# Optimization experiments

Measured on AMD Instinct MI355X. Metric: run time of the kernel, lower is better.

Reference implementation:

```python
import jax, jax.numpy as jnp
import numpy as np

# dims: batch, seq, d_model, d_hidden, routed experts, top-k, shared experts
B, S, D, H, E_R, K, E_S = 2, 1024, 1024, 512, 64, 6, 2
EPS = 1.1920929e-07  # torch.finfo(float32).eps, RMSNorm default when eps=None


def setup_inputs() -> dict:
    key = jax.random.key(0)
    ks = jax.random.split(key, 8)
    u = lambda k, shape, b: jax.random.uniform(k, shape, jnp.float32, -b, b)
    bd = 1.0 / np.sqrt(D)   # bound for W1 (1/sqrt(d_input)) and W2 (1/sqrt(d_output)=1/sqrt(D))
    bh = 1.0 / np.sqrt(H)
    return {
        "x": jax.random.normal(ks[0], (B, S, D), jnp.float32),
        "norm_w": jnp.ones((D,), jnp.float32),            # RMSNorm weight
        "Wr": u(ks[1], (E_R, D), bd),                      # router Linear weight (no bias)
        "sW1": u(ks[2], (E_S, D, H), bd), "sb1": jnp.zeros((E_S, 1, H), jnp.float32),
        "sW2": u(ks[3], (E_S, H, D), bd), "sb2": jnp.zeros((E_S, 1, D), jnp.float32),
        "sWg": u(ks[4], (H, H), bh),                       # shared-experts SwiGLU gate weight
        "rW1": u(ks[5], (E_R, D, H), bd), "rb1": jnp.zeros((E_R, 1, H), jnp.float32),
        "rW2": u(ks[6], (E_R, H, D), bd), "rb2": jnp.zeros((E_R, 1, D), jnp.float32),
        "rWg": u(ks[7], (H, H), bh),                       # routed-experts SwiGLU gate weight
        "bias": jnp.full((E_R,), 1.0 / E_R, jnp.float32), # routing bias buffer (expert_bias=True)
    }


def _rmsnorm(x, w):
    ms = jnp.mean(x * x, axis=-1, keepdims=True)
    return x * jax.lax.rsqrt(ms + EPS) * w


def _swiglu(h, Wg):
    # SwiGLU(d_model=H): silu(h @ Wg) * h, elementwise gate over hidden dim
    return jax.nn.silu(h @ Wg) * h


def reference(x, norm_w, Wr, sW1, sb1, sW2, sb2, sWg, rW1, rb1, rW2, rb2, rWg, bias):
    xn = _rmsnorm(x, norm_w)
    t = xn.reshape(-1, D)                                  # (T, D) tokens
    # --- shared experts, summed over expert axis ---
    hs = jnp.einsum('td,edh->teh', t, sW1) + sb1[None, :, 0, :]
    hs = _swiglu(hs, sWg)
    shared = jnp.einsum('teh,ehd->td', hs, sW2) + jnp.sum(sb2[:, 0, :], axis=0)
    # --- router ---
    raw = t @ Wr.T                                         # (T, E_R) raw affinity
    aff = jax.lax.stop_gradient(raw) + bias                # detached + bias for top-k selection
    _, idx = jax.lax.top_k(aff, K)                         # (T, K)
    # --- routed experts: dense all-expert FFN, gather top-k outputs ---
    # (mathematically identical to the source's per-token weight gather,
    #  but avoids materializing (T,K,D,H) weight tensors)
    h = jnp.einsum('td,edh->teh', t, rW1) + rb1[None, :, 0, :]   # (T, E_R, H)
    h = _swiglu(h, rWg)
    out_all = jnp.einsum('teh,ehd->ted', h, rW2) + rb2[None, :, 0, :]  # (T, E_R, D)
    out_k = jnp.take_along_axis(out_all, idx[:, :, None], axis=1)      # (T, K, D)
    aff_k = jnp.take_along_axis(raw, idx, axis=1)                      # (T, K) raw (undetached)
    w = aff_k / jnp.sum(aff_k, axis=-1, keepdims=True)                 # expert_bias=True path
    routed = jnp.einsum('tk,tkd->td', w, out_k)                        # (T, D)
    return x + (shared + routed).reshape(B, S, D)
```

## Files before the change

kernel.cpp:

```cpp
#include <hip/hip_runtime.h>
#include <cstdint>
#include <cstddef>

typedef unsigned short u16;
typedef unsigned int u32;
typedef __attribute__((ext_vector_type(8))) short bh8;
typedef __attribute__((ext_vector_type(4))) float fx4;

#define T_TOK 2048
#define D_DIM 1024
#define H_DIM 512
#define N_EXP 64
#define K_TOP 6
#define N_ASG (T_TOK * K_TOP)
#define R_TOT (N_ASG + 2 * T_TOK)
#define GRID_E (8 * 9 * 64)

__device__ __forceinline__ float bf2f(u16 v) {
    union { u32 u; float f; } c; c.u = ((u32)v) << 16; return c.f;
}
__device__ __forceinline__ u16 f2bf(float f) {
    union { u32 u; float f; } c; c.f = f;
    u32 u = c.u;
    return (u16)((u + 0x7fffu + ((u >> 16) & 1u)) >> 16);
}

__global__ __launch_bounds__(256) void rn4_k(
    const float* __restrict__ x, const float* __restrict__ nw,
    const float* __restrict__ Wr, float* __restrict__ raw, u16* __restrict__ xnb)
{
    int t0 = blockIdx.x << 2, tid = threadIdx.x;
    __shared__ float xs[4][D_DIM];
    __shared__ float ps[4][256];
    __shared__ float red4[4][4];
    int d0 = tid << 2;
    float4 wv = *(const float4*)(nw + d0);
    float4 xv[4];
    #pragma unroll
    for (int tt = 0; tt < 4; ++tt) {
        xv[tt] = *(const float4*)(x + (size_t)(t0 + tt) * D_DIM + d0);
        float ss = xv[tt].x * xv[tt].x + xv[tt].y * xv[tt].y
                 + xv[tt].z * xv[tt].z + xv[tt].w * xv[tt].w;
        #pragma unroll
        for (int o = 32; o > 0; o >>= 1) ss += __shfl_down(ss, o);
        if ((tid & 63) == 0) red4[tt][tid >> 6] = ss;
    }
    __syncthreads();
    #pragma unroll
    for (int tt = 0; tt < 4; ++tt) {
        float ms = (red4[tt][0] + red4[tt][1] + red4[tt][2] + red4[tt][3]) * (1.f / (float)D_DIM);
        float sc = rsqrtf(ms + 1.1920929e-07f);
        float4 xf;
        xf.x = xv[tt].x * sc * wv.x;
        xf.y = xv[tt].y * sc * wv.y;
        xf.z = xv[tt].z * sc * wv.z;
        xf.w = xv[tt].w * sc * wv.w;
        *(float4*)&xs[tt][d0] = xf;
        ushort4 ob;
        ob.x = f2bf(xf.x); ob.y = f2bf(xf.y); ob.z = f2bf(xf.z); ob.w = f2bf(xf.w);
        *(ushort4*)(xnb + (size_t)(t0 + tt) * D_DIM + d0) = ob;
    }
    __syncthreads();
    int e = tid & 63, part = tid >> 6;
    const float* wr = Wr + (size_t)e * D_DIM + part * 256;
    float s0 = 0.f, s1 = 0.f, s2 = 0.f, s3 = 0.f;
    const float* xp0 = &xs[0][part * 256];
    const float* xp1 = &xs[1][part * 256];
    const float* xp2 = &xs[2][part * 256];
    const float* xp3 = &xs[3][part * 256];
    #pragma unroll 4
    for (int i = 0; i < 256; i += 4) {
        float4 w4 = *(const float4*)(wr + i);
        s0 += xp0[i] * w4.x + xp0[i+1] * w4.y + xp0[i+2] * w4.z + xp0[i+3] * w4.w;
        s1 += xp1[i] * w4.x + xp1[i+1] * w4.y + xp1[i+2] * w4.z + xp1[i+3] * w4.w;
        s2 += xp2[i] * w4.x + xp2[i+1] * w4.y + xp2[i+2] * w4.z + xp2[i+3] * w4.w;
        s3 += xp3[i] * w4.x + xp3[i+1] * w4.y + xp3[i+2] * w4.z + xp3[i+3] * w4.w;
    }
    ps[0][tid] = s0; ps[1][tid] = s1; ps[2][tid] = s2; ps[3][tid] = s3;
    __syncthreads();
    if (part == 0) {
        #pragma unroll
        for (int tt = 0; tt < 4; ++tt)
            raw[(size_t)(t0 + tt) * N_EXP + e] =
                ps[tt][e] + ps[tt][64 + e] + ps[tt][128 + e] + ps[tt][192 + e];
    }
}

__global__ void topk_k(const float* __restrict__ raw, const float* __restrict__ ebias,
                       int* __restrict__ cnt, int* __restrict__ tki, float* __restrict__ tkw)
{
    int t = blockIdx.x, lane = threadIdx.x;
    float r = raw[(size_t)t * N_EXP + lane];
    float cur = r + ebias[lane];
    int selI[K_TOP]; float selR[K_TOP];
    #pragma unroll
    for (int k = 0; k < K_TOP; ++k) {
        float v = cur; int id = lane;
        #pragma unroll
        for (int o = 32; o > 0; o >>= 1) {
            float v2 = __shfl_down(v, o); int i2 = __shfl_down(id, o);
            if (v2 > v || (v2 == v && i2 < id)) { v = v2; id = i2; }
        }
        id = __shfl(id, 0);
        if (lane == id) cur = -3.4e38f;
        selI[k] = id;
        selR[k] = __shfl(r, id);
    }
    float s = 0.f;
    #pragma unroll
    for (int k = 0; k < K_TOP; ++k) s += selR[k];
    if (lane < K_TOP) {
        tki[t * K_TOP + lane] = selI[lane];
        tkw[t * K_TOP + lane] = selR[lane] / s;
        atomicAdd(&cnt[selI[lane]], 1);
    }
}

__global__ void scan_k(const int* __restrict__ cnt, int* __restrict__ offs, int* __restrict__ fill)
{
    int lane = threadIdx.x;
    int c = cnt[lane];
    int s = c;
    #pragma unroll
    for (int o = 1; o < 64; o <<= 1) {
        int v = __shfl_up(s, o);
        if (lane >= o) s += v;
    }
    int excl = s - c;
    offs[lane] = excl;
    fill[lane] = excl;
    if (lane == 63) offs[N_EXP] = s;
}

__global__ void fill_k(const int* __restrict__ tki, const float* __restrict__ tkw,
                       int* __restrict__ fill, int* __restrict__ atok, float* __restrict__ aw)
{
    int t = blockIdx.x, lane = threadIdx.x;
    if (lane < K_TOP) {
        int e = tki[t * K_TOP + lane];
        int p = atomicAdd(&fill[e], 1);
        atok[p] = t;
        aw[p] = tkw[t * K_TOP + lane];
    }
}

__global__ __launch_bounds__(256) void convAll_k(
    const float* __restrict__ rW1, const float* __restrict__ sW1,
    const float* __restrict__ rW2, const float* __restrict__ sW2,
    const float* __restrict__ rWg, const float* __restrict__ sWg,
    u16* __restrict__ W1f, u16* __restrict__ W2f, u16* __restrict__ Wgf)
{
    int id = blockIdx.x;
    const float* src; u16* dst;
    int K, N, n0, k0;
    const size_t MS = (size_t)H_DIM * D_DIM;
    if (id < 66 * 128) {
        int mat = id >> 7, tile = id & 127;
        K = D_DIM; N = H_DIM;
        src = (mat < N_EXP ? rW1 + (size_t)mat * MS : sW1 + (size_t)(mat - N_EXP) * MS);
        dst = W1f + (size_t)mat * MS;
        n0 = (tile & 7) << 6; k0 = (tile >> 3) << 6;
    } else if (id < 2 * 66 * 128) {
        id -= 66 * 128;
        int mat = id >> 7, tile = id & 127;
        K = H_DIM; N = D_DIM;
        src = (mat < N_EXP ? rW2 + (size_t)mat * MS : sW2 + (size_t)(mat - N_EXP) * MS);
        dst = W2f + (size_t)mat * MS;
        n0 = (tile & 15) << 6; k0 = (tile >> 4) << 6;
    } else {
        id -= 2 * 66 * 128;
        int mat = id >> 6, tile = id & 63;
        K = H_DIM; N = H_DIM;
        src = (mat == 0 ? rWg : sWg);
        dst = Wgf + (size_t)mat * (H_DIM * H_DIM);
        n0 = (tile & 7) << 6; k0 = (tile >> 3) << 6;
    }

    __shared__ u16 t[64][72];
    int tid = threadIdx.x;
    int kr = tid >> 4, c4 = (tid & 15) << 2;
    #pragma unroll
    for (int rr = 0; rr < 4; ++rr) {
        int k = (rr << 4) + kr;
        float4 v = *(const float4*)(src + (size_t)(k0 + k) * N + n0 + c4);
        t[c4 + 0][k] = f2bf(v.x);
        t[c4 + 1][k] = f2bf(v.y);
        t[c4 + 2][k] = f2bf(v.z);
        t[c4 + 3][k] = f2bf(v.w);
    }
    __syncthreads();
    int lane = tid & 63, g = tid >> 6;
    int nr = lane & 15, kq = lane >> 4;
    #pragma unroll
    for (int f = 0; f < 2; ++f) {
        int fragId = g + (f << 2);
        int ntile = fragId >> 1, kb = fragId & 1;
        bh8 v = *(const bh8*)&t[(ntile << 4) + nr][(kb << 5) + (kq << 3)];
        size_t fi = (((size_t)((n0 >> 4) + ntile) * (size_t)(K >> 5)
                      + (size_t)((k0 >> 5) + kb)) << 9) + (size_t)(lane << 3);
        *(bh8*)(dst + fi) = v;
    }
}

__device__ __forceinline__ bool slabDecode(
    int bx, const int* __restrict__ offs,
    int& e, int& rowBase, int& rows, int& tokBase)
{
    int xcd = bx & 7, rest = bx >> 3, grp = rest >> 6, slab = rest & 63;
    if (grp < 8) {
        e = (grp << 3) + xcd;
        int s0 = offs[e], s1 = offs[e + 1];
        rowBase = s0 + (slab << 5);
        if (rowBase >= s1) return false;
        rows = s1 - rowBase; if (rows > 32) rows = 32;
        tokBase = -1;
        return true;
    }
    int f = (slab << 3) + xcd;
    if (f >= 128) return false;
    int sh = f & 1;
    e = N_EXP + sh;
    tokBase = (f >> 1) << 5;
    rowBase = N_ASG + (sh << 11) + tokBase;
    rows = 32;
    return true;
}

__global__ __launch_bounds__(256, 4) void p1_k(
    const u16* __restrict__ xnb, const u16* __restrict__ W1f,
    const float* __restrict__ rb1, const float* __restrict__ sb1,
    const int* __restrict__ offs, const int* __restrict__ atok,
    u16* __restrict__ h)
{
    int e, rowBase, rows, tokBase;
    if (!slabDecode(blockIdx.x, offs, e, rowBase, rows, tokBase)) return;

    __shared__ int tok[32];
    int tid = threadIdx.x;
    if (tid < 32) {
        int cl = tid < rows ? tid : rows - 1;
        tok[tid] = (tokBase < 0) ? atok[rowBase + cl] : tokBase + tid;
    }
    __syncthreads();

    int w = tid >> 6, lane = tid & 63, quad = lane >> 4, l15 = lane & 15;
    int cg = blockIdx.y;
    int nt0 = (cg << 4) + (w << 2);
    const u16* bp = W1f + (size_t)e * (H_DIM * D_DIM)
                  + (((size_t)nt0 << 5) << 9) + (lane << 3);
    const u16* a0p = xnb + (size_t)tok[l15] * D_DIM + (quad << 3);
    const u16* a1p = xnb + (size_t)tok[16 + l15] * D_DIM + (quad << 3);
    const float* b1 = (tokBase < 0) ? rb1 + e * H_DIM : sb1 + (e - N_EXP) * H_DIM;

    fx4 ac0[4] = {}, ac1[4] = {};
    bh8 bA[4], bB[4], aA0, aA1, aB0, aB1;
    #pragma unroll
    for (int ct = 0; ct < 4; ++ct) bA[ct] = *(const bh8*)(bp + ((size_t)(ct << 5) << 9));
    aA0 = *(const bh8*)a0p; aA1 = *(const bh8*)a1p;
    #pragma unroll 1
    for (int kb = 0; kb < 32; kb += 2) {
        #pragma unroll
        for (int ct = 0; ct < 4; ++ct) bB[ct] = *(const bh8*)(bp + (((ct << 5) + kb + 1) << 9));
        aB0 = *(const bh8*)(a0p + ((kb + 1) << 5));
        aB1 = *(const bh8*)(a1p + ((kb + 1) << 5));
        #pragma unroll
        for (int ct = 0; ct < 4; ++ct) {
            ac0[ct] = __builtin_amdgcn_mfma_f32_16x16x32_bf16(aA0, bA[ct], ac0[ct], 0, 0, 0);
            ac1[ct] = __builtin_amdgcn_mfma_f32_16x16x32_bf16(aA1, bA[ct], ac1[ct], 0, 0, 0);
        }
        #pragma unroll
        for (int ct = 0; ct < 4; ++ct) bA[ct] = *(const bh8*)(bp + (((ct << 5) + kb + 2) << 9));
        aA0 = *(const bh8*)(a0p + ((kb + 2) << 5));
        aA1 = *(const bh8*)(a1p + ((kb + 2) << 5));
        #pragma unroll
        for (int ct = 0; ct < 4; ++ct) {
            ac0[ct] = __builtin_amdgcn_mfma_f32_16x16x32_bf16(aB0, bB[ct], ac0[ct], 0, 0, 0);
            ac1[ct] = __builtin_amdgcn_mfma_f32_16x16x32_bf16(aB1, bB[ct], ac1[ct], 0, 0, 0);
        }
    }
    #pragma unroll
    for (int ct = 0; ct < 4; ++ct) {
        int col = ((nt0 + ct) << 4) + l15;
        float bv = b1[col];
        #pragma unroll
        for (int r = 0; r < 4; ++r) {
            int r0 = (quad << 2) + r;
            if (r0 < rows) h[(size_t)(rowBase + r0) * H_DIM + col] = f2bf(ac0[ct][r] + bv);
            int r1 = 16 + r0;
            if (r1 < rows) h[(size_t)(rowBase + r1) * H_DIM + col] = f2bf(ac1[ct][r] + bv);
        }
    }
}

__global__ __launch_bounds__(256, 4) void p2_k(
    const u16* __restrict__ hbuf, const u16* __restrict__ Wgf, u16* __restrict__ hg)
{
    int rowBase = blockIdx.x << 5;
    int tid = threadIdx.x;
    int w = tid >> 6, lane = tid & 63, quad = lane >> 4, l15 = lane & 15;
    int cg = blockIdx.y;
    int nt0 = (cg << 4) + (w << 2);
    const u16* bp = Wgf + (rowBase < N_ASG ? 0 : (size_t)(H_DIM * H_DIM))
                  + (((size_t)nt0 << 4) << 9) + (lane << 3);
    const u16* a0p = hbuf + (size_t)(rowBase + l15) * H_DIM + (quad << 3);
    const u16* a1p = hbuf + (size_t)(rowBase + 16 + l15) * H_DIM + (quad << 3);

    fx4 ac0[4] = {}, ac1[4] = {};
    bh8 bA[4], bB[4], aA0, aA1, aB0, aB1;
    #pragma unroll
    for (int ct = 0; ct < 4; ++ct) bA[ct] = *(const bh8*)(bp + ((size_t)(ct << 4) << 9));
    aA0 = *(const bh8*)a0p; aA1 = *(const bh8*)a1p;
    #pragma unroll 1
    for (int kb = 0; kb < 16; kb += 2) {
        #pragma unroll
        for (int ct = 0; ct < 4; ++ct) bB[ct] = *(const bh8*)(bp + (((ct << 4) + kb + 1) << 9));
        aB0 = *(const bh8*)(a0p + ((kb + 1) << 5));
        aB1 = *(const bh8*)(a1p + ((kb + 1) << 5));
        #pragma unroll
        for (int ct = 0; ct < 4; ++ct) {
            ac0[ct] = __builtin_amdgcn_mfma_f32_16x16x32_bf16(aA0, bA[ct], ac0[ct], 0, 0, 0);
            ac1[ct] = __builtin_amdgcn_mfma_f32_16x16x32_bf16(aA1, bA[ct], ac1[ct], 0, 0, 0);
        }
        #pragma unroll
        for (int ct = 0; ct < 4; ++ct) bA[ct] = *(const bh8*)(bp + (((ct << 4) + kb + 2) << 9));
        aA0 = *(const bh8*)(a0p + ((kb + 2) << 5));
        aA1 = *(const bh8*)(a1p + ((kb + 2) << 5));
        #pragma unroll
        for (int ct = 0; ct < 4; ++ct) {
            ac0[ct] = __builtin_amdgcn_mfma_f32_16x16x32_bf16(aB0, bB[ct], ac0[ct], 0, 0, 0);
            ac1[ct] = __builtin_amdgcn_mfma_f32_16x16x32_bf16(aB1, bB[ct], ac1[ct], 0, 0, 0);
        }
    }
    #pragma unroll
    for (int ct = 0; ct < 4; ++ct) {
        int col = ((nt0 + ct) << 4) + l15;
        #pragma unroll
        for (int r = 0; r < 4; ++r) {
            int r0 = (quad << 2) + r;
            size_t i0 = (size_t)(rowBase + r0) * H_DIM + col;
            float g0 = ac0[ct][r], h0 = bf2f(hbuf[i0]);
            hg[i0] = f2bf(h0 * g0 * (1.f / (1.f + __expf(-g0))));
            int r1 = 16 + r0;
            size_t i1 = (size_t)(rowBase + r1) * H_DIM + col;
            float g1 = ac1[ct][r], h1 = bf2f(hbuf[i1]);
            hg[i1] = f2bf(h1 * g1 * (1.f / (1.f + __expf(-g1))));
        }
    }
}

__global__ __launch_bounds__(256, 4) void p3_k(
    const u16* __restrict__ hg, const u16* __restrict__ W2f,
    const float* __restrict__ rb2, const float* __restrict__ sb2,
    const int* __restrict__ offs, const int* __restrict__ atok,
    const float* __restrict__ aw, float* __restrict__ accG)
{
    int e, rowBase, rows, tokBase;
    if (!slabDecode(blockIdx.x, offs, e, rowBase, rows, tokBase)) return;

    __shared__ int tok[32];
    __shared__ float wt[32];
    int tid = threadIdx.x;
    if (tid < 32) {
        int cl = tid < rows ? tid : rows - 1;
        if (tokBase < 0) { tok[tid] = atok[rowBase + cl]; wt[tid] = aw[rowBase + cl]; }
        else             { tok[tid] = tokBase + tid;      wt[tid] = 1.0f; }
    }
    __syncthreads();

    int w = tid >> 6, lane = tid & 63, quad = lane >> 4, l15 = lane & 15;
    int cg = blockIdx.y;
    int nt0 = (cg << 4) + (w << 2);
    const u16* bp = W2f + (size_t)e * (H_DIM * D_DIM)
                  + (((size_t)nt0 << 4) << 9) + (lane << 3);
    const u16* a0p = hg + (size_t)(rowBase + l15) * H_DIM + (quad << 3);
    const u16* a1p = hg + (size_t)(rowBase + 16 + l15) * H_DIM + (quad << 3);
    const float* b2 = (tokBase < 0) ? rb2 + e * D_DIM : sb2 + (e - N_EXP) * D_DIM;

    fx4 ac0[4] = {}, ac1[4] = {};
    bh8 bA[4], bB[4], aA0, aA1, aB0, aB1;
    #pragma unroll
    for (int ct = 0; ct < 4; ++ct) bA[ct] = *(const bh8*)(bp + ((size_t)(ct << 4) << 9));
    aA0 = *(const bh8*)a0p; aA1 = *(const bh8*)a1p;
    #pragma unroll 1
    for (int kb = 0; kb < 16; kb += 2) {
        #pragma unroll
        for (int ct = 0; ct < 4; ++ct) bB[ct] = *(const bh8*)(bp + (((ct << 4) + kb + 1) << 9));
        aB0 = *(const bh8*)(a0p + ((kb + 1) << 5));
        aB1 = *(const bh8*)(a1p + ((kb + 1) << 5));
        #pragma unroll
        for (int ct = 0; ct < 4; ++ct) {
            ac0[ct] = __builtin_amdgcn_mfma_f32_16x16x32_bf16(aA0, bA[ct], ac0[ct], 0, 0, 0);
            ac1[ct] = __builtin_amdgcn_mfma_f32_16x16x32_bf16(aA1, bA[ct], ac1[ct], 0, 0, 0);
        }
        #pragma unroll
        for (int ct = 0; ct < 4; ++ct) bA[ct] = *(const bh8*)(bp + (((ct << 4) + kb + 2) << 9));
        aA0 = *(const bh8*)(a0p + ((kb + 2) << 5));
        aA1 = *(const bh8*)(a1p + ((kb + 2) << 5));
        #pragma unroll
        for (int ct = 0; ct < 4; ++ct) {
            ac0[ct] = __builtin_amdgcn_mfma_f32_16x16x32_bf16(aB0, bB[ct], ac0[ct], 0, 0, 0);
            ac1[ct] = __builtin_amdgcn_mfma_f32_16x16x32_bf16(aB1, bB[ct], ac1[ct], 0, 0, 0);
        }
    }
    #pragma unroll
    for (int ct = 0; ct < 4; ++ct) {
        int col = ((nt0 + ct) << 4) + l15;
        float bv = b2[col];
        #pragma unroll
        for (int r = 0; r < 4; ++r) {
            int r0 = (quad << 2) + r;
            if (r0 < rows)
                atomicAdd(&accG[(size_t)tok[r0] * D_DIM + col], wt[r0] * (ac0[ct][r] + bv));
            int r1 = 16 + r0;
            if (r1 < rows)
                atomicAdd(&accG[(size_t)tok[r1] * D_DIM + col], wt[r1] * (ac1[ct][r] + bv));
        }
    }
}

template<int ROUTED>
__global__ __launch_bounds__(256) void moe_ffn_k(
    const u16* __restrict__ xnb,
    const float* __restrict__ W1b, const float* __restrict__ Wg,
    const float* __restrict__ W2b,
    const float* __restrict__ b1b, const float* __restrict__ b2b,
    const int* __restrict__ offs, const int* __restrict__ atok,
    const float* __restrict__ aw, float* __restrict__ accG)
{
    int e = blockIdx.z;
    int start = ROUTED ? offs[e] : 0;
    int end   = ROUTED ? offs[e + 1] : T_TOK;
    int rowBase = start + (blockIdx.y << 5);
    if (rowBase >= end) return;
    int rows = end - rowBase; if (rows > 32) rows = 32;

    __shared__ int   tok[32];
    __shared__ float wt[32];
    __shared__ u16 hA[32 * 520];
    __shared__ u16 hG[32 * 520];
    __shared__ u16 As[32 * 32];
    __shared__ u16 Bs[64 * 36];

    int tid = threadIdx.x;
    if (tid < 32) {
        int cl = rowBase + tid; if (cl >= end) cl = end - 1;
        tok[tid] = ROUTED ? atok[cl] : cl;
        wt[tid]  = ROUTED ? aw[cl] : 1.0f;
    }
    __syncthreads();

    const float* W1 = W1b + (size_t)e * (D_DIM * H_DIM);
    const float* W2 = W2b + (size_t)e * (D_DIM * H_DIM);
    const float* b1 = b1b + e * H_DIM;
    const float* b2 = b2b + e * D_DIM;

    int w = tid >> 6, lane = tid & 63, quad = lane >> 4, l15 = lane & 15;
    int sr2 = tid >> 3, sc2 = (tid & 7) << 2;

    for (int nc = 0; nc < 8; ++nc) {
        int n0 = nc << 6;
        fx4 a0 = {}; fx4 a1 = {};
        for (int kc = 0; kc < 32; ++kc) {
            int kb = kc << 5;
            int2 av = *(const int2*)(xnb + (size_t)tok[sr2] * D_DIM + kb + sc2);
            const float* cp = W1 + n0 + lane;
            int kx = kb + (w << 3);
            u32 p[4];
            #pragma unroll
            for (int jj = 0; jj < 4; ++jj) {
                u32 lo = f2bf(cp[(size_t)(kx + 2 * jj) * H_DIM]);
                u32 hi = f2bf(cp[(size_t)(kx + 2 * jj + 1) * H_DIM]);
                p[jj] = lo | (hi << 16);
            }
            __syncthreads();
            *(int2*)&As[sr2 * 32 + sc2] = av;
            u16* bsw = &Bs[lane * 36 + (w << 3)];
            uint2 q0; q0.x = p[0]; q0.y = p[1];
            uint2 q1; q1.x = p[2]; q1.y = p[3];
            *(uint2*)bsw = q0;
            *(uint2*)(bsw + 4) = q1;
            __syncthreads();
            bh8 af0 = *(const bh8*)&As[l15 * 32 + (quad << 3)];
            bh8 af1 = *(const bh8*)&As[(16 + l15) * 32 + (quad << 3)];
            const u16* brp = &Bs[((w << 4) + l15) * 36 + (quad << 3)];
            union { bh8 v; uint2 u2[2]; } bf;
            bf.u2[0] = *(const uint2*)brp;
            bf.u2[1] = *(const uint2*)(brp + 4);
            a0 = __builtin_amdgcn_mfma_f32_16x16x32_bf16(af0, bf.v, a0, 0, 0, 0);
            a1 = __builtin_amdgcn_mfma_f32_16x16x32_bf16(af1, bf.v, a1, 0, 0, 0);
        }
        int col = n0 + (w << 4) + l15;
        float bv = b1[col];
        #pragma unroll
        for (int r = 0; r < 4; ++r) {
            hA[((quad << 2) + r) * 520 + col]      = f2bf(a0[r] + bv);
            hA[(16 + (quad << 2) + r) * 520 + col] = f2bf(a1[r] + bv);
        }
    }
    __syncthreads();

    for (int nc = 0; nc < 8; ++nc) {
        int n0 = nc << 6;
        fx4 a0 = {}; fx4 a1 = {};
        for (int kc = 0; kc < 16; ++kc) {
            int kb = kc << 5;
            const float* cp = Wg + n0 + lane;
            int kx = kb + (w << 3);
            u32 p[4];
            #pragma unroll
            for (int jj = 0; jj < 4; ++jj) {
                u32 lo = f2bf(cp[(size_t)(kx + 2 * jj) * H_DIM]);
                u32 hi = f2bf(cp[(size_t)(kx + 2 * jj + 1) * H_DIM]);
                p[jj] = lo | (hi << 16);
            }
            __syncthreads();
            u16* bsw = &Bs[lane * 36 + (w << 3)];
            uint2 q0; q0.x = p[0]; q0.y = p[1];
            uint2 q1; q1.x = p[2]; q1.y = p[3];
            *(uint2*)bsw = q0;
            *(uint2*)(bsw + 4) = q1;
            __syncthreads();
            bh8 af0 = *(const bh8*)&hA[l15 * 520 + kb + (quad << 3)];
            bh8 af1 = *(const bh8*)&hA[(16 + l15) * 520 + kb + (quad << 3)];
            const u16* brp = &Bs[((w << 4) + l15) * 36 + (quad << 3)];
            union { bh8 v; uint2 u2[2]; } bf;
            bf.u2[0] = *(const uint2*)brp;
            bf.u2[1] = *(const uint2*)(brp + 4);
            a0 = __builtin_amdgcn_mfma_f32_16x16x32_bf16(af0, bf.v, a0, 0, 0, 0);
            a1 = __builtin_amdgcn_mfma_f32_16x16x32_bf16(af1, bf.v, a1, 0, 0, 0);
        }
        int col = n0 + (w << 4) + l15;
        #pragma unroll
        for (int r = 0; r < 4; ++r) {
            int r0 = (quad << 2) + r;
            float h0 = bf2f(hA[r0 * 520 + col]);
            float g0 = a0[r];
            hG[r0 * 520 + col] = f2bf(h0 * g0 * (1.f / (1.f + __expf(-g0))));
            int r1 = 16 + r0;
            float h1 = bf2f(hA[r1 * 520 + col]);
            float g1 = a1[r];
            hG[r1 * 520 + col] = f2bf(h1 * g1 * (1.f / (1.f + __expf(-g1))));
        }
    }
    __syncthreads();

    for (int nc = 0; nc < 16; ++nc) {
        int n0 = nc << 6;
        fx4 a0 = {}; fx4 a1 = {};
        for (int kc = 0; kc < 16; ++kc) {
            int kb = kc << 5;
            const float* cp = W2 + n0 + lane;
            int kx = kb + (w << 3);
            u32 p[4];
            #pragma unroll
            for (int jj = 0; jj < 4; ++jj) {
                u32 lo = f2bf(cp[(size_t)(kx + 2 * jj) * D_DIM]);
                u32 hi = f2bf(cp[(size_t)(kx + 2 * jj + 1) * D_DIM]);
                p[jj] = lo | (hi << 16);
            }
            __syncthreads();
            u16* bsw = &Bs[lane * 36 + (w << 3)];
            uint2 q0; q0.x = p[0]; q0.y = p[1];
            uint2 q1; q1.x = p[2]; q1.y = p[3];
            *(uint2*)bsw = q0;
            *(uint2*)(bsw + 4) = q1;
            __syncthreads();
            bh8 af0 = *(const bh8*)&hG[l15 * 520 + kb + (quad << 3)];
            bh8 af1 = *(const bh8*)&hG[(16 + l15) * 520 + kb + (quad << 3)];
            const u16* brp = &Bs[((w << 4) + l15) * 36 + (quad << 3)];
            union { bh8 v; uint2 u2[2]; } bf;
            bf.u2[0] = *(const uint2*)brp;
            bf.u2[1] = *(const uint2*)(brp + 4);
            a0 = __builtin_amdgcn_mfma_f32_16x16x32_bf16(af0, bf.v, a0, 0, 0, 0);
            a1 = __builtin_amdgcn_mfma_f32_16x16x32_bf16(af1, bf.v, a1, 0, 0, 0);
        }
        int col = n0 + (w << 4) + l15;
        float bv = b2[col];
        #pragma unroll
        for (int r = 0; r < 4; ++r) {
            int lr0 = (quad << 2) + r;
            if (lr0 < rows)
                atomicAdd(&accG[(size_t)tok[lr0] * D_DIM + col], wt[lr0] * (a0[r] + bv));
            int lr1 = 16 + lr0;
            if (lr1 < rows)
                atomicAdd(&accG[(size_t)tok[lr1] * D_DIM + col], wt[lr1] * (a1[r] + bv));
        }
    }
}

__global__ __launch_bounds__(256) void final_k(
    const float* __restrict__ x, const float* __restrict__ acc, float* __restrict__ out)
{
    size_t i = ((size_t)blockIdx.x * 256 + threadIdx.x) << 2;
    float4 xv = *(const float4*)(x + i);
    float4 a = *(const float4*)(acc + i);
    float4 o;
    o.x = xv.x + a.x;
    o.y = xv.y + a.y;
    o.z = xv.z + a.z;
    o.w = xv.w + a.w;
    *(float4*)(out + i) = o;
}

extern "C" void kernel_launch(void* const* d_in, const int* in_sizes, int n_in,
                              void* d_out, int out_size, void* d_ws, size_t ws_size,
                              hipStream_t stream)
{
    const float* x     = (const float*)d_in[0];
    const float* nw    = (const float*)d_in[1];
    const float* Wr    = (const float*)d_in[2];
    const float* sW1   = (const float*)d_in[3];
    const float* sb1   = (const float*)d_in[4];
    const float* sW2   = (const float*)d_in[5];
    const float* sb2   = (const float*)d_in[6];
    const float* sWg   = (const float*)d_in[7];
    const float* rW1   = (const float*)d_in[8];
    const float* rb1   = (const float*)d_in[9];
    const float* rW2   = (const float*)d_in[10];
    const float* rb2   = (const float*)d_in[11];
    const float* rWg   = (const float*)d_in[12];
    const float* ebias = (const float*)d_in[13];
    float* out = (float*)d_out;
    (void)in_sizes; (void)n_in; (void)out_size;

    char* wp = (char*)d_ws;
    auto alloc = [&](size_t b) { char* p = wp; wp += (b + 255) & ~(size_t)255; return p; };
    int*   cnt  = (int*)alloc(N_EXP * 4);
    int*   offs = (int*)alloc((N_EXP + 1) * 4);
    int*   fill = (int*)alloc(N_EXP * 4);
    int*   tki  = (int*)alloc((size_t)T_TOK * K_TOP * 4);
    float* tkw  = (float*)alloc((size_t)T_TOK * K_TOP * 4);
    int*   atok = (int*)alloc((size_t)N_ASG * 4);
    float* aw   = (float*)alloc((size_t)N_ASG * 4);
    float* raw  = (float*)alloc((size_t)T_TOK * N_EXP * 4);
    u16*   xnb  = (u16*)alloc((size_t)T_TOK * D_DIM * 2);
    float* acc  = (float*)alloc((size_t)T_TOK * D_DIM * 4);
    u16* W1f = (u16*)alloc((size_t)(N_EXP + 2) * H_DIM * D_DIM * 2);
    u16* W2f = (u16*)alloc((size_t)(N_EXP + 2) * H_DIM * D_DIM * 2);
    u16* Wgf = (u16*)alloc((size_t)2 * H_DIM * H_DIM * 2);
    u16* h   = (u16*)alloc((size_t)R_TOT * H_DIM * 2);
    u16* hg  = (u16*)alloc((size_t)R_TOT * H_DIM * 2);
    alloc(1 << 16);
    bool fast = (size_t)(wp - (char*)d_ws) <= ws_size;

    hipMemsetAsync(cnt, 0, N_EXP * 4, stream);
    hipMemsetAsync(acc, 0, (size_t)T_TOK * D_DIM * 4, stream);

    dim3 b256(256);
    rn4_k<<<T_TOK / 4, b256, 0, stream>>>(x, nw, Wr, raw, xnb);
    topk_k<<<T_TOK, dim3(64), 0, stream>>>(raw, ebias, cnt, tki, tkw);
    scan_k<<<1, dim3(64), 0, stream>>>(cnt, offs, fill);
    fill_k<<<T_TOK, dim3(64), 0, stream>>>(tki, tkw, fill, atok, aw);

    if (fast) {
        convAll_k<<<dim3(2 * 66 * 128 + 2 * 64), b256, 0, stream>>>(
            rW1, sW1, rW2, sW2, rWg, sWg, W1f, W2f, Wgf);

        p1_k<<<dim3(GRID_E, 2), b256, 0, stream>>>(xnb, W1f, rb1, sb1, offs, atok, h);
        p2_k<<<dim3(R_TOT / 32, 2), b256, 0, stream>>>(h, Wgf, hg);
        p3_k<<<dim3(GRID_E, 4), b256, 0, stream>>>(hg, W2f, rb2, sb2, offs, atok, aw, acc);
    } else {
        moe_ffn_k<1><<<dim3(1, 64, N_EXP), b256, 0, stream>>>(
            xnb, rW1, rWg, rW2, rb1, rb2, offs, atok, aw, acc);
        moe_ffn_k<0><<<dim3(1, 64, 2), b256, 0, stream>>>(
            xnb, sW1, sWg, sW2, sb1, sb2, offs, atok, aw, acc);
    }

    final_k<<<(T_TOK * D_DIM) / 1024, b256, 0, stream>>>(x, acc, out);
}
```

Baseline: 651.6 us.

## Replace atomic scatter with per-row output buffer and deterministic gather reduction

The down-projection kernel now writes each weighted expert row to a dense per-assignment buffer instead of doing float atomicAdds into a token accumulator. A new gather kernel sums the six routed rows and two shared rows per token and adds the residual. This removes the accumulator memset and the final kernel, at the cost of a large extra fp32 buffer round trip through memory. The gate kernel is also reshaped to 16-row tiles covering all 512 columns in one block and updates h in place, which drops the separate hg buffer. The LDS transpose padding in the weight conversion kernel changes from 72 to 68.

```diff
diff --git a/kernel.cpp b/kernel.cpp
--- a/kernel.cpp
+++ b/kernel.cpp
@@ -133,7 +133,8 @@
 }
 
 __global__ void fill_k(const int* __restrict__ tki, const float* __restrict__ tkw,
-                       int* __restrict__ fill, int* __restrict__ atok, float* __restrict__ aw)
+                       int* __restrict__ fill, int* __restrict__ atok, float* __restrict__ aw,
+                       int* __restrict__ rowOf)
 {
     int t = blockIdx.x, lane = threadIdx.x;
     if (lane < K_TOP) {
@@ -141,6 +142,7 @@
         int p = atomicAdd(&fill[e], 1);
         atok[p] = t;
         aw[p] = tkw[t * K_TOP + lane];
+        rowOf[t * K_TOP + lane] = p;
     }
 }
 
@@ -176,7 +178,7 @@
         n0 = (tile & 7) << 6; k0 = (tile >> 3) << 6;
     }
 
-    __shared__ u16 t[64][72];
+    __shared__ u16 t[64][68];
     int tid = threadIdx.x;
     int kr = tid >> 4, c4 = (tid & 15) << 2;
     #pragma unroll
@@ -293,66 +295,57 @@
 }
 
 __global__ __launch_bounds__(256, 4) void p2_k(
-    const u16* __restrict__ hbuf, const u16* __restrict__ Wgf, u16* __restrict__ hg)
-{
-    int rowBase = blockIdx.x << 5;
+    u16* __restrict__ h, const u16* __restrict__ Wgf)
+{
+    int rowBase = blockIdx.x << 4;
     int tid = threadIdx.x;
     int w = tid >> 6, lane = tid & 63, quad = lane >> 4, l15 = lane & 15;
-    int cg = blockIdx.y;
-    int nt0 = (cg << 4) + (w << 2);
-    const u16* bp = Wgf + (rowBase < N_ASG ? 0 : (size_t)(H_DIM * H_DIM))
-                  + (((size_t)nt0 << 4) << 9) + (lane << 3);
-    const u16* a0p = hbuf + (size_t)(rowBase + l15) * H_DIM + (quad << 3);
-    const u16* a1p = hbuf + (size_t)(rowBase + 16 + l15) * H_DIM + (quad << 3);
-
-    fx4 ac0[4] = {}, ac1[4] = {};
-    bh8 bA[4], bB[4], aA0, aA1, aB0, aB1;
-    #pragma unroll
-    for (int ct = 0; ct < 4; ++ct) bA[ct] = *(const bh8*)(bp + ((size_t)(ct << 4) << 9));
-    aA0 = *(const bh8*)a0p; aA1 = *(const bh8*)a1p;
+    const u16* bp = Wgf + (rowBase < N_ASG ? 0 : (size_t)(H_DIM * H_DIM)) + (lane << 3);
+    const u16* a0p = h + (size_t)(rowBase + l15) * H_DIM + (quad << 3);
+
+    fx4 ac[8] = {};
+    bh8 bA[8], bB[8], aA, aB;
+    #pragma unroll
+    for (int ct = 0; ct < 8; ++ct)
+        bA[ct] = *(const bh8*)(bp + ((((size_t)(w << 3) + ct) << 4) << 9));
+    aA = *(const bh8*)a0p;
     #pragma unroll 1
     for (int kb = 0; kb < 16; kb += 2) {
         #pragma unroll
-        for (int ct = 0; ct < 4; ++ct) bB[ct] = *(const bh8*)(bp + (((ct << 4) + kb + 1) << 9));
-        aB0 = *(const bh8*)(a0p + ((kb + 1) << 5));
-        aB1 = *(const bh8*)(a1p + ((kb + 1) << 5));
-        #pragma unroll
-        for (int ct = 0; ct < 4; ++ct) {
-            ac0[ct] = __builtin_amdgcn_mfma_f32_16x16x32_bf16(aA0, bA[ct], ac0[ct], 0, 0, 0);
-            ac1[ct] = __builtin_amdgcn_mfma_f32_16x16x32_bf16(aA1, bA[ct], ac1[ct], 0, 0, 0);
-        }
-        #pragma unroll
-        for (int ct = 0; ct < 4; ++ct) bA[ct] = *(const bh8*)(bp + (((ct << 4) + kb + 2) << 9));
-        aA0 = *(const bh8*)(a0p + ((kb + 2) << 5));
-        aA1 = *(const bh8*)(a1p + ((kb + 2) << 5));
-        #pragma unroll
-        for (int ct = 0; ct < 4; ++ct) {
-            ac0[ct] = __builtin_amdgcn_mfma_f32_16x16x32_bf16(aB0, bB[ct], ac0[ct], 0, 0, 0);
-            ac1[ct] = __builtin_amdgcn_mfma_f32_16x16x32_bf16(aB1, bB[ct], ac1[ct], 0, 0, 0);
-        }
-    }
-    #pragma unroll
-    for (int ct = 0; ct < 4; ++ct) {
-        int col = ((nt0 + ct) << 4) + l15;
+        for (int ct = 0; ct < 8; ++ct)
+            bB[ct] = *(const bh8*)(bp + (((((size_t)(w << 3) + ct) << 4) + kb + 1) << 9));
+        aB = *(const bh8*)(a0p + ((kb + 1) << 5));
+        #pragma unroll
+        for (int ct = 0; ct < 8; ++ct)
+            ac[ct] = __builtin_amdgcn_mfma_f32_16x16x32_bf16(aA, bA[ct], ac[ct], 0, 0, 0);
+        #pragma unroll
+        for (int ct = 0; ct < 8; ++ct)
+            bA[ct] = *(const bh8*)(bp + (((((size_t)(w << 3) + ct) << 4) + kb + 2) << 9));
+        aA = *(const bh8*)(a0p + ((kb + 2) << 5));
+        #pragma unroll
+        for (int ct = 0; ct < 8; ++ct)
+            ac[ct] = __builtin_amdgcn_mfma_f32_16x16x32_bf16(aB, bB[ct], ac[ct], 0, 0, 0);
+    }
+    __syncthreads();
+    #pragma unroll
+    for (int ct = 0; ct < 8; ++ct) {
+        int col = (((w << 3) + ct) << 4) + l15;
         #pragma unroll
         for (int r = 0; r < 4; ++r) {
-            int r0 = (quad << 2) + r;
-            size_t i0 = (size_t)(rowBase + r0) * H_DIM + col;
-            float g0 = ac0[ct][r], h0 = bf2f(hbuf[i0]);
-            hg[i0] = f2bf(h0 * g0 * (1.f / (1.f + __expf(-g0))));
-            int r1 = 16 + r0;
-            size_t i1 = (size_t)(rowBase + r1) * H_DIM + col;
-            float g1 = ac1[ct][r], h1 = bf2f(hbuf[i1]);
-            hg[i1] = f2bf(h1 * g1 * (1.f / (1.f + __expf(-g1))));
-        }
-    }
-}
-
+            int row = rowBase + (quad << 2) + r;
+            size_t i = (size_t)row * H_DIM + col;
+            float g = ac[ct][r], hv = bf2f(h[i]);
+            h[i] = f2bf(hv * g * (1.f / (1.f + __expf(-g))));
+        }
+    }
+}
+
+template<int ATOM>
 __global__ __launch_bounds__(256, 4) void p3_k(
     const u16* __restrict__ hg, const u16* __restrict__ W2f,
     const float* __restrict__ rb2, const float* __restrict__ sb2,
     const int* __restrict__ offs, const int* __restrict__ atok,
-    const float* __restrict__ aw, float* __restrict__ accG)
+    const float* __restrict__ aw, float* __restrict__ accG, float* __restrict__ outAll)
 {
     int e, rowBase, rows, tokBase;
     if (!slabDecode(blockIdx.x, offs, e, rowBase, rows, tokBase)) return;
@@ -409,13 +402,43 @@
         #pragma unroll
         for (int r = 0; r < 4; ++r) {
             int r0 = (quad << 2) + r;
-            if (r0 < rows)
-                atomicAdd(&accG[(size_t)tok[r0] * D_DIM + col], wt[r0] * (ac0[ct][r] + bv));
+            if (r0 < rows) {
+                float v = wt[r0] * (ac0[ct][r] + bv);
+                if (ATOM) atomicAdd(&accG[(size_t)tok[r0] * D_DIM + col], v);
+                else      outAll[(size_t)(rowBase + r0) * D_DIM + col] = v;
+            }
             int r1 = 16 + r0;
-            if (r1 < rows)
-                atomicAdd(&accG[(size_t)tok[r1] * D_DIM + col], wt[r1] * (ac1[ct][r] + bv));
-        }
-    }
+            if (r1 < rows) {
+                float v = wt[r1] * (ac1[ct][r] + bv);
+                if (ATOM) atomicAdd(&accG[(size_t)tok[r1] * D_DIM + col], v);
+                else      outAll[(size_t)(rowBase + r1) * D_DIM + col] = v;
+            }
+        }
+    }
+}
+
+__global__ __launch_bounds__(256) void gather_k(
+    const float* __restrict__ x, const float* __restrict__ outAll,
+    const int* __restrict__ rowOf, float* __restrict__ out)
+{
+    int t = blockIdx.x, tid = threadIdx.x;
+    __shared__ int rws[K_TOP];
+    if (tid < K_TOP) rws[tid] = rowOf[t * K_TOP + tid];
+    __syncthreads();
+    int d0 = tid << 2;
+    size_t base = (size_t)t * D_DIM + d0;
+    float4 xv = *(const float4*)(x + base);
+    float4 s = *(const float4*)(outAll + (size_t)(N_ASG + t) * D_DIM + d0);
+    float4 s1 = *(const float4*)(outAll + (size_t)(N_ASG + T_TOK + t) * D_DIM + d0);
+    s.x += s1.x; s.y += s1.y; s.z += s1.z; s.w += s1.w;
+    #pragma unroll
+    for (int k = 0; k < K_TOP; ++k) {
+        float4 v = *(const float4*)(outAll + (size_t)rws[k] * D_DIM + d0);
+        s.x += v.x; s.y += v.y; s.z += v.z; s.w += v.w;
+    }
+    float4 o;
+    o.x = xv.x + s.x; o.y = xv.y + s.y; o.z = xv.z + s.z; o.w = xv.w + s.w;
+    *(float4*)(out + base) = o;
 }
 
 template<int ROUTED>
@@ -632,6 +655,7 @@
     float* tkw  = (float*)alloc((size_t)T_TOK * K_TOP * 4);
     int*   atok = (int*)alloc((size_t)N_ASG * 4);
     float* aw   = (float*)alloc((size_t)N_ASG * 4);
+    int*   rowOf= (int*)alloc((size_t)T_TOK * K_TOP * 4);
     float* raw  = (float*)alloc((size_t)T_TOK * N_EXP * 4);
     u16*   xnb  = (u16*)alloc((size_t)T_TOK * D_DIM * 2);
     float* acc  = (float*)alloc((size_t)T_TOK * D_DIM * 4);
@@ -639,32 +663,44 @@
     u16* W2f = (u16*)alloc((size_t)(N_EXP + 2) * H_DIM * D_DIM * 2);
     u16* Wgf = (u16*)alloc((size_t)2 * H_DIM * H_DIM * 2);
     u16* h   = (u16*)alloc((size_t)R_TOT * H_DIM * 2);
-    u16* hg  = (u16*)alloc((size_t)R_TOT * H_DIM * 2);
     alloc(1 << 16);
-    bool fast = (size_t)(wp - (char*)d_ws) <= ws_size;
+    char* markA = wp;
+    float* outAll = (float*)alloc((size_t)R_TOT * D_DIM * 4);
+    char* markB = wp;
+    bool fastA = (size_t)(markA - (char*)d_ws) <= ws_size;
+    bool fast2 = (size_t)(markB - (char*)d_ws) <= ws_size;
 
     hipMemsetAsync(cnt, 0, N_EXP * 4, stream);
-    hipMemsetAsync(acc, 0, (size_t)T_TOK * D_DIM * 4, stream);
 
     dim3 b256(256);
     rn4_k<<<T_TOK / 4, b256, 0, stream>>>(x, nw, Wr, raw, xnb);
     topk_k<<<T_TOK, dim3(64), 0, stream>>>(raw, ebias, cnt, tki, tkw);
     scan_k<<<1, dim3(64), 0, stream>>>(cnt, offs, fill);
-    fill_k<<<T_TOK, dim3(64), 0, stream>>>(tki, tkw, fill, atok, aw);
-
-    if (fast) {
+    fill_k<<<T_TOK, dim3(64), 0, stream>>>(tki, tkw, fill, atok, aw, rowOf);
+
+    if (fast2) {
         convAll_k<<<dim3(2 * 66 * 128 + 2 * 64), b256, 0, stream>>>(
             rW1, sW1, rW2, sW2, rWg, sWg, W1f, W2f, Wgf);
-
         p1_k<<<dim3(GRID_E, 2), b256, 0, stream>>>(xnb, W1f, rb1, sb1, offs, atok, h);
-        p2_k<<<dim3(R_TOT / 32, 2), b256, 0, stream>>>(h, Wgf, hg);
-        p3_k<<<dim3(GRID_E, 4), b256, 0, stream>>>(hg, W2f, rb2, sb2, offs, atok, aw, acc);
+        p2_k<<<dim3(R_TOT / 16), b256, 0, stream>>>(h, Wgf);
+        p3_k<0><<<dim3(GRID_E, 4), b256, 0, stream>>>(
+            h, W2f, rb2, sb2, offs, atok, aw, nullptr, outAll);
+        gather_k<<<T_TOK, b256, 0, stream>>>(x, outAll, rowOf, out);
+    } else if (fastA) {
+        hipMemsetAsync(acc, 0, (size_t)T_TOK * D_DIM * 4, stream);
+        convAll_k<<<dim3(2 * 66 * 128 + 2 * 64), b256, 0, stream>>>(
+            rW1, sW1, rW2, sW2, rWg, sWg, W1f, W2f, Wgf);
+        p1_k<<<dim3(GRID_E, 2), b256, 0, stream>>>(xnb, W1f, rb1, sb1, offs, atok, h);
+        p2_k<<<dim3(R_TOT / 16), b256, 0, stream>>>(h, Wgf);
+        p3_k<1><<<dim3(GRID_E, 4), b256, 0, stream>>>(
+            h, W2f, rb2, sb2, offs, atok, aw, acc, nullptr);
+        final_k<<<(T_TOK * D_DIM) / 1024, b256, 0, stream>>>(x, acc, out);
     } else {
+        hipMemsetAsync(acc, 0, (size_t)T_TOK * D_DIM * 4, stream);
         moe_ffn_k<1><<<dim3(1, 64, N_EXP), b256, 0, stream>>>(
             xnb, rW1, rWg, rW2, rb1, rb2, offs, atok, aw, acc);
         moe_ffn_k<0><<<dim3(1, 64, 2), b256, 0, stream>>>(
             xnb, sW1, sWg, sW2, sb1, sb2, offs, atok, aw, acc);
-    }
-
-    final_k<<<(T_TOK * D_DIM) / 1024, b256, 0, stream>>>(x, acc, out);
-}
+        final_k<<<(T_TOK * D_DIM) / 1024, b256, 0, stream>>>(x, acc, out);
+    }
+}
```

After: 638.6 us. -2.0%, faster.
